# Performance work log

Hardware: AMD Instinct MI355X
Metric: run time of the kernel (lower is better)

The kernel has to match this reference:

```python
import jax, jax.numpy as jnp
import numpy as np

N_NODES = 10000
IN_F = 512
OUT_F = 512
N_EDGES = 160000
GRID_SIZE = 5      # KAN spline grid intervals
SPLINE_ORDER = 3   # cubic B-splines -> GRID_SIZE + SPLINE_ORDER = 8 basis fns per input dim
ALPHA = 0.2        # LeakyReLU negative slope


def _grid():
    # uniform extended grid on [-1, 1], shape [GRID_SIZE + 2*SPLINE_ORDER + 1]
    step = 2.0 / GRID_SIZE
    return jnp.arange(-SPLINE_ORDER, GRID_SIZE + SPLINE_ORDER + 1, dtype=jnp.float32) * step - 1.0


def _b_splines(x, grid):
    # x: [N, in] -> basis: [N, in, GRID_SIZE + SPLINE_ORDER] via Cox-de Boor recursion
    x = x[..., None]  # [N, in, 1]
    bases = ((x >= grid[:-1]) & (x < grid[1:])).astype(x.dtype)  # order-0
    for p in range(1, SPLINE_ORDER + 1):
        left = (x - grid[: -(p + 1)]) / (grid[p:-1] - grid[: -(p + 1)]) * bases[..., :-1]
        right = (grid[p + 1:] - x) / (grid[p + 1:] - grid[1:-p]) * bases[..., 1:]
        bases = left + right
    return bases


def setup_inputs() -> dict:
    key = jax.random.key(0)
    k1, k2, k3, k4, k5, k6 = jax.random.split(key, 6)
    h = jax.random.normal(k1, (N_NODES, IN_F), dtype=jnp.float32)
    edge_index = jax.random.randint(k2, (2, N_EDGES), 0, N_NODES, dtype=jnp.int64)
    xav = float(np.sqrt(2.0 / (IN_F + OUT_F))) * 1.414
    W = jax.random.normal(k3, (IN_F, OUT_F), dtype=jnp.float32) * xav
    a = jax.random.normal(k4, (2 * OUT_F, 1), dtype=jnp.float32) * float(np.sqrt(2.0 / (2 * OUT_F + 1)))
    base_w = jax.random.normal(k5, (OUT_F, IN_F), dtype=jnp.float32) * xav
    n_coef = GRID_SIZE + SPLINE_ORDER
    spline_w = jax.random.normal(k6, (OUT_F, IN_F, n_coef), dtype=jnp.float32) * 0.1
    return {"h": h, "W": W, "a": a, "base_w": base_w, "spline_w": spline_w, "edge_index": edge_index}


def reference(h, W, a, base_w, spline_w, edge_index):
    HW = h @ W  # [N, out]
    row, col = edge_index[0], edge_index[1]
    # a_input @ a == HW_i @ a[:out] + HW_j @ a[out:] (same math, avoids the concat)
    s = HW @ a[:OUT_F, 0]   # [N]
    t = HW @ a[OUT_F:, 0]   # [N]
    e = jax.nn.leaky_relu(s[row] + t[col], negative_slope=ALPHA)  # [E]
    # segment softmax keyed on destination (row)
    m = jax.ops.segment_max(e, row, num_segments=N_NODES)
    ex = jnp.exp(e - m[row])
    den = jax.ops.segment_sum(ex, row, num_segments=N_NODES)
    att = ex / den[row]
    # dropout p=0.6 is identity in eval mode
    # scatter-add aggregation of raw features h[col] (as in the source)
    agg = jax.ops.segment_sum(att[:, None] * h[col], row, num_segments=N_NODES)  # [N, in]
    # KANLayer: silu base path + B-spline path (efficient-KAN formulation)
    grid = _grid()
    basis = _b_splines(agg, grid)  # [N, in, n_coef]
    out = jax.nn.silu(agg) @ base_w.T + jnp.einsum('nip,oip->no', basis, spline_w)
    return out
```

## Files before the change

kernel.cpp:

```cpp
#include <hip/hip_runtime.h>
#include <hip/hip_bf16.h>
#include <math.h>

#define N_NODES 10000
#define IN_F 512
#define OUT_F 512
#define N_EDGES 160000
#define K_SPLINE 4096
#define K_TOTAL 4608
#define NBK 144
#define NBM 628
#define ALPHA 0.2f

typedef __attribute__((ext_vector_type(8))) short short8;
typedef __attribute__((ext_vector_type(4))) float f32x4;
typedef unsigned short ushort_t;
typedef unsigned long long u64;

__device__ __forceinline__ unsigned bfpair(float a, float b) {
    __hip_bfloat162 h2 = __float22bfloat162_rn(make_float2(a, b));
    return *reinterpret_cast<unsigned*>(&h2);
}
__device__ __forceinline__ float bflo(unsigned u) { return __uint_as_float(u << 16); }
__device__ __forceinline__ float bfhi(unsigned u) { return __uint_as_float(u & 0xffff0000u); }

__device__ __forceinline__ float silu_f(float x) {
    return x / (1.f + __expf(-x));
}

__device__ __forceinline__ uint4 spline_window(float x) {
    float xc = (x + 2.2f) * 2.5f;
    float fc = floorf(xc);
    int c = (int)fc;
    float u = xc - fc;
    float omu = 1.f - u;
    float u2 = u * u, u3 = u2 * u;
    float n0 = (1.f / 6.f) * omu * omu * omu;
    float n1 = 0.5f * u3 - u2 + (2.f / 3.f);
    float n2 = -0.5f * u3 + 0.5f * u2 + 0.5f * u + (1.f / 6.f);
    float n3 = (1.f / 6.f) * u3;
    u64 V = (u64)bfpair(n0, n1) | ((u64)bfpair(n2, n3) << 32);
    int sh = (c - 3) * 16;
    u64 lo, hi;
    if (c < 0 || c > 10)    { lo = 0; hi = 0; }
    else if (sh >= 64)      { lo = 0; hi = V << (sh - 64); }
    else if (sh > 0)        { lo = V << sh; hi = V >> (64 - sh); }
    else if (sh == 0)       { lo = V; hi = 0; }
    else                    { lo = V >> (-sh); hi = 0; }
    uint4 pk;
    pk.x = (unsigned)lo; pk.y = (unsigned)(lo >> 32);
    pk.z = (unsigned)hi; pk.w = (unsigned)(hi >> 32);
    return pk;
}

__global__ void wa_deg_kernel(const float* __restrict__ W, const float* __restrict__ a,
                              float* __restrict__ wa0, float* __restrict__ wa1,
                              int* __restrict__ deg) {
    int b = blockIdx.x;
    int tid = threadIdx.x;
    if (b < 128) {
        int w = tid >> 6, l = tid & 63;
        int i = b * 4 + w;
        float s0 = 0.f, s1 = 0.f;
        #pragma unroll
        for (int oo = 0; oo < 8; ++oo) {
            int o = l + oo * 64;
            float wv = W[(size_t)i * OUT_F + o];
            s0 += wv * a[o];
            s1 += wv * a[OUT_F + o];
        }
        #pragma unroll
        for (int off = 32; off > 0; off >>= 1) {
            s0 += __shfl_down(s0, off, 64);
            s1 += __shfl_down(s1, off, 64);
        }
        if (l == 0) { wa0[i] = s0; wa1[i] = s1; }
    } else {
        int idx = (b - 128) * 256 + tid;
        if (idx < N_NODES) deg[idx] = 0;
    }
}

__global__ void fused1_kernel(const float* __restrict__ h, ushort_t* __restrict__ hb,
                              const float* __restrict__ wa0, const float* __restrict__ wa1,
                              float* __restrict__ s, float* __restrict__ t,
                              const float* __restrict__ base_w, const float* __restrict__ spline_w,
                              ushort_t* __restrict__ Bt,
                              const int* __restrict__ ei, int* __restrict__ deg) {
    int b = blockIdx.x;
    int tid = threadIdx.x;
    if (b < 625) {
        int k = b * 256 + tid;
        if (k < N_EDGES) atomicAdd(&deg[ei[k]], 1);
    } else if (b < 3125) {
        int bb = b - 625;
        int w = tid >> 6, l = tid & 63;
        int n = bb * 4 + w;
        const float* hp = h + (size_t)n * IN_F + l * 8;
        float4 x0 = *(const float4*)hp;
        float4 x1 = *(const float4*)(hp + 4);
        uint4 pk;
        pk.x = bfpair(x0.x, x0.y);
        pk.y = bfpair(x0.z, x0.w);
        pk.z = bfpair(x1.x, x1.y);
        pk.w = bfpair(x1.z, x1.w);
        *(uint4*)(hb + (size_t)n * IN_F + l * 8) = pk;
        const float4* w0 = (const float4*)(wa0 + l * 8);
        const float4* w1 = (const float4*)(wa1 + l * 8);
        float4 a0 = w0[0], a1 = w0[1];
        float4 b0 = w1[0], b1 = w1[1];
        float ss = x0.x*a0.x + x0.y*a0.y + x0.z*a0.z + x0.w*a0.w
                 + x1.x*a1.x + x1.y*a1.y + x1.z*a1.z + x1.w*a1.w;
        float tt = x0.x*b0.x + x0.y*b0.y + x0.z*b0.z + x0.w*b0.w
                 + x1.x*b1.x + x1.y*b1.y + x1.z*b1.z + x1.w*b1.w;
        #pragma unroll
        for (int o = 32; o > 0; o >>= 1) {
            ss += __shfl_down(ss, o, 64);
            tt += __shfl_down(tt, o, 64);
        }
        if (l == 0) { s[n] = ss; t[n] = tt; }
    } else {
        int gid = (b - 3125) * 256 + tid;
        int o = gid / 576;
        int kb8 = gid - o * 576;
        int k0 = kb8 * 8;
        float4 x0, x1;
        if (k0 < K_SPLINE) {
            const float4* p = (const float4*)(spline_w + (size_t)o * K_SPLINE + k0);
            x0 = p[0]; x1 = p[1];
        } else {
            const float4* p = (const float4*)(base_w + (size_t)o * IN_F + (k0 - K_SPLINE));
            x0 = p[0]; x1 = p[1];
        }
        int frag = (k0 >> 5) * 32 + (o >> 4);
        int lane = ((kb8 & 3) << 4) + (o & 15);
        uint4 pk;
        pk.x = bfpair(x0.x, x0.y);
        pk.y = bfpair(x0.z, x0.w);
        pk.z = bfpair(x1.x, x1.y);
        pk.w = bfpair(x1.z, x1.w);
        *(uint4*)(Bt + ((size_t)frag * 64 + lane) * 8) = pk;
    }
}

__global__ void scan_kernel(const int* __restrict__ deg, int* __restrict__ off,
                            int* __restrict__ cursor) {
    __shared__ int sb[256];
    int tid = threadIdx.x;
    int d[40];
    int tot = 0;
    #pragma unroll
    for (int j = 0; j < 40; ++j) {
        int idx = tid * 40 + j;
        d[j] = (idx < N_NODES) ? deg[idx] : 0;
        tot += d[j];
    }
    sb[tid] = tot;
    __syncthreads();
    for (int sd = 1; sd < 256; sd <<= 1) {
        int v = (tid >= sd) ? sb[tid - sd] : 0;
        __syncthreads();
        sb[tid] += v;
        __syncthreads();
    }
    int run = (tid > 0) ? sb[tid - 1] : 0;
    #pragma unroll
    for (int j = 0; j < 40; ++j) {
        int idx = tid * 40 + j;
        if (idx < N_NODES) { off[idx] = run; cursor[idx] = run; }
        run += d[j];
    }
    if (tid == 255) off[N_NODES] = sb[255];
}

__global__ void fill_kernel(const int* __restrict__ ei, int* __restrict__ cursor,
                            int* __restrict__ csr_col) {
    int k = blockIdx.x * 256 + threadIdx.x;
    if (k < N_EDGES) {
        int r = ei[k];
        int c = ei[N_EDGES + k];
        int p = atomicAdd(&cursor[r], 1);
        csr_col[p] = c;
    }
}

__global__ __launch_bounds__(256) void agg_kernel(
    const ushort_t* __restrict__ hb, const float* __restrict__ s,
    const float* __restrict__ t, const int* __restrict__ off,
    const int* __restrict__ csr, float* __restrict__ agg) {
    int w = threadIdx.x >> 6, l = threadIdx.x & 63;
    int n = blockIdx.x * 4 + w;
    int e0 = off[n], e1 = off[n + 1];
    float sn = s[n];

    float m = -1e30f, den = 0.f;
    for (int k = e0 + l; k < e1; k += 64) {
        float v = sn + t[csr[k]];
        v = (v >= 0.f) ? v : ALPHA * v;
        float mn = fmaxf(m, v);
        den = den * __expf(m - mn) + __expf(v - mn);
        m = mn;
    }
    #pragma unroll
    for (int o = 1; o < 64; o <<= 1) {
        float m2 = __shfl_xor(m, o, 64);
        float d2 = __shfl_xor(den, o, 64);
        float mn = fmaxf(m, m2);
        den = den * __expf(m - mn) + d2 * __expf(m2 - mn);
        m = mn;
    }
    float inv = (den > 0.f) ? 1.f / den : 0.f;

    int hl = l >> 5;
    int lo = l & 31;
    float acc[16];
    #pragma unroll
    for (int i = 0; i < 16; ++i) acc[i] = 0.f;
    const ushort_t* hbl = hb + lo * 16;

    for (int base = e0; base < e1; base += 64) {
        int cnt = e1 - base; if (cnt > 64) cnt = 64;
        int c = 0; float att = 0.f;
        if (l < cnt) {
            c = csr[base + l];
            float v = sn + t[c];
            v = (v >= 0.f) ? v : ALPHA * v;
            att = __expf(v - m) * inv;
        }
        int npair = (cnt + 1) >> 1;
        #pragma unroll 2
        for (int j = 0; j < npair; ++j) {
            int e = 2 * j + hl;
            float aj = __shfl(att, e, 64);
            int cj = __shfl(c, e, 64);
            const ushort_t* rp = hbl + (size_t)cj * IN_F;
            uint4 u0 = *(const uint4*)rp;
            uint4 u1 = *(const uint4*)(rp + 8);
            acc[0]  = fmaf(aj, bflo(u0.x), acc[0]);
            acc[1]  = fmaf(aj, bfhi(u0.x), acc[1]);
            acc[2]  = fmaf(aj, bflo(u0.y), acc[2]);
            acc[3]  = fmaf(aj, bfhi(u0.y), acc[3]);
            acc[4]  = fmaf(aj, bflo(u0.z), acc[4]);
            acc[5]  = fmaf(aj, bfhi(u0.z), acc[5]);
            acc[6]  = fmaf(aj, bflo(u0.w), acc[6]);
            acc[7]  = fmaf(aj, bfhi(u0.w), acc[7]);
            acc[8]  = fmaf(aj, bflo(u1.x), acc[8]);
            acc[9]  = fmaf(aj, bfhi(u1.x), acc[9]);
            acc[10] = fmaf(aj, bflo(u1.y), acc[10]);
            acc[11] = fmaf(aj, bfhi(u1.y), acc[11]);
            acc[12] = fmaf(aj, bflo(u1.z), acc[12]);
            acc[13] = fmaf(aj, bfhi(u1.z), acc[13]);
            acc[14] = fmaf(aj, bflo(u1.w), acc[14]);
            acc[15] = fmaf(aj, bfhi(u1.w), acc[15]);
        }
    }
    #pragma unroll
    for (int i = 0; i < 16; ++i) acc[i] += __shfl_xor(acc[i], 32, 64);

    if (hl == 0) {
        float* arow = agg + (size_t)n * IN_F + lo * 16;
        *(float4*)(arow)      = make_float4(acc[0],  acc[1],  acc[2],  acc[3]);
        *(float4*)(arow + 4)  = make_float4(acc[4],  acc[5],  acc[6],  acc[7]);
        *(float4*)(arow + 8)  = make_float4(acc[8],  acc[9],  acc[10], acc[11]);
        *(float4*)(arow + 12) = make_float4(acc[12], acc[13], acc[14], acc[15]);
    }
}

__global__ __launch_bounds__(256) void expand_kernel(const float* __restrict__ agg,
                                                     ushort_t* __restrict__ Xf) {
    __shared__ float AL[16][516];
    int nb = blockIdx.x;
    int tid = threadIdx.x;

    #pragma unroll
    for (int i = 0; i < 8; ++i) {
        int idx = i * 256 + tid;
        int r = idx >> 7, c4 = idx & 127;
        int n = nb * 16 + r;
        float4 v = (n < N_NODES) ? ((const float4*)(agg + (size_t)n * IN_F))[c4]
                                 : make_float4(0.f, 0.f, 0.f, 0.f);
        *(float4*)&AL[r][c4 * 4] = v;
    }
    __syncthreads();

    int w = tid >> 6, l = tid & 63;
    bool live = (nb * 16 + (l & 15)) < N_NODES;
    #pragma unroll 1
    for (int i = 0; i < 36; ++i) {
        int kb = w + 4 * i;
        uint4 pk = make_uint4(0u, 0u, 0u, 0u);
        if (live) {
            if (kb < 128) {
                int dim = kb * 4 + (l >> 4);
                pk = spline_window(AL[l & 15][dim]);
            } else {
                const float* ap = &AL[l & 15][(kb - 128) * 32 + (l >> 4) * 8];
                float4 x0 = *(const float4*)ap;
                float4 x1 = *(const float4*)(ap + 4);
                pk.x = bfpair(silu_f(x0.x), silu_f(x0.y));
                pk.y = bfpair(silu_f(x0.z), silu_f(x0.w));
                pk.z = bfpair(silu_f(x1.x), silu_f(x1.y));
                pk.w = bfpair(silu_f(x1.z), silu_f(x1.w));
            }
        }
        *(uint4*)(Xf + ((size_t)(nb * NBK + kb) * 64 + l) * 8) = pk;
    }
}

__global__ __launch_bounds__(256, 3) void kan_gemm2(
    const ushort_t* __restrict__ Xf, const ushort_t* __restrict__ Bt,
    float* __restrict__ out) {
    __shared__ ushort_t A_lds[2][4][4][64][8];

    int d = blockIdx.x;
    int g = d >> 5, r = d & 31;
    int bm = g * 8 + (r & 7), bn = r >> 3;
    if (bm >= 157) return;
    int tid = threadIdx.x, w = tid >> 6, l = tid & 63;
    int wc16 = bn * 8 + w * 2;

    f32x4 acc[4][2];
    #pragma unroll
    for (int m = 0; m < 4; ++m)
        #pragma unroll
        for (int nf = 0; nf < 2; ++nf)
            acc[m][nf] = (f32x4){0.f, 0.f, 0.f, 0.f};

    short8 b0[8], b1[8];

    auto stage = [&](int j, int pb) {
        #pragma unroll
        for (int ks = 0; ks < 4; ++ks) {
            const ushort_t* src = Xf + (((size_t)(bm * 4 + w) * NBK + 4 * j + ks) * 64 + l) * 8;
            __builtin_amdgcn_global_load_lds(
                (const __attribute__((address_space(1))) unsigned int*)src,
                (__attribute__((address_space(3))) unsigned int*)&A_lds[pb][ks][w][0][0],
                16, 0, 0);
        }
    };
    auto loadB = [&](int j, short8 (&b)[8]) {
        #pragma unroll
        for (int ks = 0; ks < 4; ++ks) {
            int kb = 4 * j + ks;
            b[ks * 2 + 0] = *(const short8*)(Bt + ((size_t)(kb * 32 + wc16)     * 64 + l) * 8);
            b[ks * 2 + 1] = *(const short8*)(Bt + ((size_t)(kb * 32 + wc16 + 1) * 64 + l) * 8);
        }
    };
    auto compute = [&](int pb, short8 (&b)[8]) {
        #pragma unroll
        for (int ks = 0; ks < 4; ++ks)
            #pragma unroll
            for (int m = 0; m < 4; ++m) {
                short8 af = *(const short8*)&A_lds[pb][ks][m][l][0];
                acc[m][0] = __builtin_amdgcn_mfma_f32_16x16x32_bf16(af, b[ks * 2 + 0], acc[m][0], 0, 0, 0);
                acc[m][1] = __builtin_amdgcn_mfma_f32_16x16x32_bf16(af, b[ks * 2 + 1], acc[m][1], 0, 0, 0);
            }
    };

    stage(0, 0);
    loadB(0, b0);
    __syncthreads();
    for (int j = 0; j < 36; j += 2) {
        if (j + 1 < 36) { stage(j + 1, 1); loadB(j + 1, b1); }
        compute(0, b0);
        __syncthreads();
        if (j + 2 < 36) { stage(j + 2, 0); loadB(j + 2, b0); }
        compute(1, b1);
        __syncthreads();
    }

    #pragma unroll
    for (int m = 0; m < 4; ++m) {
        int r0 = bm * 64 + m * 16 + ((l >> 4) << 2);
        #pragma unroll
        for (int nf = 0; nf < 2; ++nf) {
            int colg = bn * 128 + w * 32 + nf * 16 + (l & 15);
            #pragma unroll
            for (int jr = 0; jr < 4; ++jr) {
                int rr = r0 + jr;
                if (rr < N_NODES) out[(size_t)rr * OUT_F + colg] = acc[m][nf][jr];
            }
        }
    }
}

extern "C" void kernel_launch(void* const* d_in, const int* in_sizes, int n_in,
                              void* d_out, int out_size, void* d_ws, size_t ws_size,
                              hipStream_t stream) {
    const float* h        = (const float*)d_in[0];
    const float* W        = (const float*)d_in[1];
    const float* a        = (const float*)d_in[2];
    const float* base_w   = (const float*)d_in[3];
    const float* spline_w = (const float*)d_in[4];
    const int*   ei       = (const int*)d_in[5];
    float* out = (float*)d_out;

    char* ws = (char*)d_ws;
    size_t cur = 0;
    auto alloc = [&](size_t bytes) -> void* {
        void* p = ws + cur;
        cur += (bytes + 255) & ~(size_t)255;
        return p;
    };
    float* wa0    = (float*)alloc(512 * 4);
    float* wa1    = (float*)alloc(512 * 4);
    float* s      = (float*)alloc(N_NODES * 4);
    float* t      = (float*)alloc(N_NODES * 4);
    int*   deg    = (int*)alloc(N_NODES * 4);
    int*   offp   = (int*)alloc((N_NODES + 1) * 4);
    int*   cursor = (int*)alloc(N_NODES * 4);
    int*   csr    = (int*)alloc(N_EDGES * 4);
    float* agg    = (float*)alloc((size_t)N_NODES * IN_F * 4);
    ushort_t* Bt  = (ushort_t*)alloc((size_t)K_TOTAL * OUT_F * 2);
    ushort_t* hb  = (ushort_t*)alloc((size_t)N_NODES * IN_F * 2);
    ushort_t* Xf  = (ushort_t*)alloc((size_t)NBM * NBK * 64 * 16);
    if (cur > ws_size) return;

    wa_deg_kernel<<<168, 256, 0, stream>>>(W, a, wa0, wa1, deg);
    fused1_kernel<<<4277, 256, 0, stream>>>(h, hb, wa0, wa1, s, t, base_w, spline_w, Bt, ei, deg);
    scan_kernel<<<1, 256, 0, stream>>>(deg, offp, cursor);
    fill_kernel<<<625, 256, 0, stream>>>(ei, cursor, csr);
    agg_kernel<<<2500, 256, 0, stream>>>(hb, s, t, offp, csr, agg);
    expand_kernel<<<628, 256, 0, stream>>>(agg, Xf);
    kan_gemm2<<<640, 256, 0, stream>>>(Xf, Bt, out);
}
```

Measured before the change: 161.1 us.

## Triple-buffer A tiles in LDS with explicit vmcnt waits and one barrier

Converts the GEMM main loop from double-buffered LDS staging with two __syncthreads per pair of iterations to a three-stage LDS ring. Each iteration issues a manual s_waitcnt vmcnt and a single s_barrier, which keeps two A-tile loads in flight while the current tile is computed. The intent is to hide global-to-LDS latency better and cut barrier overhead. The cost is 50% more LDS per block, which may lower occupancy. Correctness also depends on the hand-counted vmcnt values matching the number of outstanding loads.

Result: no change. 161.4 us (+0.2%).

```diff
diff --git a/kernel.cpp b/kernel.cpp
--- a/kernel.cpp
+++ b/kernel.cpp
@@ -16,6 +16,8 @@
 typedef __attribute__((ext_vector_type(4))) float f32x4;
 typedef unsigned short ushort_t;
 typedef unsigned long long u64;
+
+#define WAITVM(N) asm volatile("s_waitcnt vmcnt(" #N ")" ::: "memory")
 
 __device__ __forceinline__ unsigned bfpair(float a, float b) {
     __hip_bfloat162 h2 = __float22bfloat162_rn(make_float2(a, b));
@@ -310,7 +312,7 @@
 __global__ __launch_bounds__(256, 3) void kan_gemm2(
     const ushort_t* __restrict__ Xf, const ushort_t* __restrict__ Bt,
     float* __restrict__ out) {
-    __shared__ ushort_t A_lds[2][4][4][64][8];
+    __shared__ ushort_t A_lds[3][4][4][64][8];
 
     int d = blockIdx.x;
     int g = d >> 5, r = d & 31;
@@ -326,9 +328,10 @@
         for (int nf = 0; nf < 2; ++nf)
             acc[m][nf] = (f32x4){0.f, 0.f, 0.f, 0.f};
 
-    short8 b0[8], b1[8];
-
-    auto stage = [&](int j, int pb) {
+    short8 breg[2][8];
+
+    auto stage = [&](int j) {
+        int pb = j % 3;
         #pragma unroll
         for (int ks = 0; ks < 4; ++ks) {
             const ushort_t* src = Xf + (((size_t)(bm * 4 + w) * NBK + 4 * j + ks) * 64 + l) * 8;
@@ -338,7 +341,8 @@
                 16, 0, 0);
         }
     };
-    auto loadB = [&](int j, short8 (&b)[8]) {
+    auto loadB = [&](int j) {
+        short8* b = breg[j % 2];
         #pragma unroll
         for (int ks = 0; ks < 4; ++ks) {
             int kb = 4 * j + ks;
@@ -346,7 +350,9 @@
             b[ks * 2 + 1] = *(const short8*)(Bt + ((size_t)(kb * 32 + wc16 + 1) * 64 + l) * 8);
         }
     };
-    auto compute = [&](int pb, short8 (&b)[8]) {
+    auto compute = [&](int j) {
+        int pb = j % 3;
+        short8* b = breg[j % 2];
         #pragma unroll
         for (int ks = 0; ks < 4; ++ks)
             #pragma unroll
@@ -357,16 +363,17 @@
             }
     };
 
-    stage(0, 0);
-    loadB(0, b0);
-    __syncthreads();
-    for (int j = 0; j < 36; j += 2) {
-        if (j + 1 < 36) { stage(j + 1, 1); loadB(j + 1, b1); }
-        compute(0, b0);
-        __syncthreads();
-        if (j + 2 < 36) { stage(j + 2, 0); loadB(j + 2, b0); }
-        compute(1, b1);
-        __syncthreads();
+    stage(0); stage(1); loadB(0);
+
+    #pragma unroll 6
+    for (int j = 0; j < 36; ++j) {
+        if (j < 35) { WAITVM(12); }
+        else        { WAITVM(8);  }
+        __builtin_amdgcn_s_barrier();
+        __builtin_amdgcn_sched_barrier(0);
+        if (j + 1 < 36) loadB(j + 1);
+        if (j + 2 < 36) stage(j + 2);
+        compute(j);
     }
 
     #pragma unroll
```
